# Kernel tuning notes

Hardware: AMD Instinct MI355X
Metric: run time of the kernel (lower is better)

## Reference

```python
import jax, jax.numpy as jnp
import numpy as np
import math

B, L, D_IN = 4, 8192, 64
H = 256          # d_model
N2 = 32          # d_state // 2 complex conjugate pairs (S4D)
NL = 4           # n_layers
D_OUT = 10


def setup_inputs() -> dict:
    key = jax.random.key(0)
    ks = jax.random.split(key, 16)
    x = jax.random.normal(ks[0], (B, L, D_IN), dtype=jnp.float32)
    # encoder Linear(d_input, d_model)
    enc_W = jax.random.normal(ks[1], (H, D_IN), dtype=jnp.float32) / np.sqrt(D_IN)
    enc_b = jnp.zeros((H,), dtype=jnp.float32)
    # per-layer S4D parameters (stacked over n_layers)
    log_dt = jax.random.uniform(ks[2], (NL, H), dtype=jnp.float32,
                                minval=math.log(1e-3), maxval=math.log(1e-1))
    log_A_re = jnp.full((NL, H, N2), math.log(0.5), dtype=jnp.float32)
    A_im = jnp.tile(math.pi * jnp.arange(N2, dtype=jnp.float32), (NL, H, 1))
    C_re = jax.random.normal(ks[3], (NL, H, N2), dtype=jnp.float32) * (0.5 ** 0.5)
    C_im = jax.random.normal(ks[4], (NL, H, N2), dtype=jnp.float32) * (0.5 ** 0.5)
    D = jax.random.normal(ks[5], (NL, H), dtype=jnp.float32)
    # S4 block output linear (H -> 2H) followed by GLU
    Wo = jax.random.normal(ks[6], (NL, 2 * H, H), dtype=jnp.float32) / np.sqrt(H)
    bo = jnp.zeros((NL, 2 * H), dtype=jnp.float32)
    # post-norm LayerNorm over d_model
    ln_w = jnp.ones((NL, H), dtype=jnp.float32)
    ln_b = jnp.zeros((NL, H), dtype=jnp.float32)
    # final decoder Linear(d_model, d_output)
    out_W = jax.random.normal(ks[7], (D_OUT, H), dtype=jnp.float32) / np.sqrt(H)
    out_b = jnp.zeros((D_OUT,), dtype=jnp.float32)
    return dict(x=x, enc_W=enc_W, enc_b=enc_b, log_dt=log_dt, log_A_re=log_A_re,
                A_im=A_im, C_re=C_re, C_im=C_im, D=D, Wo=Wo, bo=bo,
                ln_w=ln_w, ln_b=ln_b, out_W=out_W, out_b=out_b)


def _s4d_kernel(log_dt, log_A_re, A_im, C_re, C_im, L):
    # S4D-ZOH-ish (S4D-Lin) kernel: K[h,l] = 2 Re sum_n C~[h,n] exp(l*dt*A[h,n])
    dt = jnp.exp(log_dt)[:, None]                      # (H,1)
    A = -jnp.exp(log_A_re) + 1j * A_im                 # (H,N2)
    dtA = dt * A                                       # (H,N2)
    Ct = (C_re + 1j * C_im) * (jnp.exp(dtA) - 1.0) / A # (H,N2)
    t = jnp.arange(L, dtype=jnp.float32)
    V = jnp.exp(dtA[:, :, None] * t)                   # (H,N2,L) Vandermonde
    return 2.0 * jnp.einsum('hn,hnl->hl', Ct, V).real  # (H,L)


def reference(x, enc_W, enc_b, log_dt, log_A_re, A_im, C_re, C_im, D, Wo, bo,
              ln_w, ln_b, out_W, out_b):
    Bc, Lc, _ = x.shape
    h = x @ enc_W.T + enc_b          # (B,L,H)
    h = h.transpose(0, 2, 1)         # (B,H,L) (transposed layout)
    n_layers = log_dt.shape[0]
    for i in range(n_layers):
        K = _s4d_kernel(log_dt[i], log_A_re[i], A_im[i], C_re[i], C_im[i], Lc)
        # FFT convolution (causal, non-circular via 2L padding)
        Kf = jnp.fft.rfft(K, n=2 * Lc)                       # (H, L+1)
        hf = jnp.fft.rfft(h, n=2 * Lc)                       # (B,H,L+1)
        y = jnp.fft.irfft(hf * Kf, n=2 * Lc)[..., :Lc]
        y = y + D[i][:, None] * h                            # skip D*u
        y = jax.nn.gelu(y)
        # output linear (H -> 2H) + GLU, pointwise over length
        u = jnp.einsum('oh,bhl->bol', Wo[i], y) + bo[i][:, None]
        Hd = h.shape[1]
        z = u[:, :Hd] * jax.nn.sigmoid(u[:, Hd:])
        h = z + h                                            # residual
        # post-norm LayerNorm over channel (d_model) dim
        mu = h.mean(axis=1, keepdims=True)
        var = h.var(axis=1, keepdims=True)
        h = (h - mu) / jnp.sqrt(var + 1e-5) * ln_w[i][:, None] + ln_b[i][:, None]
    h = h.transpose(0, 2, 1)          # (B,L,H)
    return h @ out_W.T + out_b        # (B,L,d_output)
```

## Files before the change

kernel.cpp:

```cpp
#include <hip/hip_runtime.h>
#include <hip/hip_bf16.h>


constexpr int B_ = 4, L_ = 8192, DIN = 64, H_ = 256, N2_ = 32, NL_ = 4, DOUT = 10;
constexpr int LC = 64, CHK = L_ / LC;
constexpr int GCH = B_ * CHK;
constexpr int M_ = B_ * L_;

constexpr size_t OFF_WOB  = 8388608;
constexpr size_t OFF_PW   = 8650752;
constexpr size_t OFF_PCT  = 8716288;
constexpr size_t OFF_PWLC = 8781824;
constexpr size_t OFF_PZ   = 8847360;
constexpr size_t OFF_EWT  = 8912896;
constexpr size_t OFF_UCM  = 8929280;
constexpr size_t OFF_YCM  = 13123584;
constexpr size_t OFF_MT   = 21512192;
constexpr size_t OFF_MW   = 22036480;
constexpr size_t OFF_MV   = 22560768;

typedef short bf16x8 __attribute__((ext_vector_type(8)));
typedef short short8 __attribute__((ext_vector_type(8)));
typedef float f32x4  __attribute__((ext_vector_type(4)));
typedef int   int2v  __attribute__((ext_vector_type(2)));

__device__ __forceinline__ float b2f(short s) {
    union { float f; unsigned u; } c;
    c.u = ((unsigned)(unsigned short)s) << 16;
    return c.f;
}

__global__ __launch_bounds__(256) void k_params(
    const float* __restrict__ log_dt, const float* __restrict__ log_A_re,
    const float* __restrict__ A_im, const float* __restrict__ C_re,
    const float* __restrict__ C_im, float* __restrict__ ws)
{
    int idx = blockIdx.x * 256 + threadIdx.x;
    if (idx >= NL_ * H_ * N2_) return;
    int i  = idx / (H_ * N2_);
    int hh = (idx / N2_) % H_;
    float dt  = expf(log_dt[i * H_ + hh]);
    float Are = -expf(log_A_re[idx]);
    float Aim = A_im[idx];
    float zre = dt * Are, zim = dt * Aim;
    float er  = expf(zre);
    float wre = er * cosf(zim), wim = er * sinf(zim);
    float d   = Are * Are + Aim * Aim;
    float nre = wre - 1.f, nim = wim;
    float qre = (nre * Are + nim * Aim) / d;
    float qim = (nim * Are - nre * Aim) / d;
    float cr = C_re[idx], ci = C_im[idx];
    float ctre = cr * qre - ci * qim;
    float ctim = cr * qim + ci * qre;
    float er2 = expf(zre * (float)LC);
    float wlre = er2 * cosf(zim * (float)LC);
    float wlim = er2 * sinf(zim * (float)LC);
    ((float2*)(ws + OFF_PW))[idx]   = make_float2(wre, wim);
    ((float2*)(ws + OFF_PCT))[idx]  = make_float2(2.f * ctre, 2.f * ctim);
    ((float2*)(ws + OFF_PWLC))[idx] = make_float2(wlre, wlim);
    ((float2*)(ws + OFF_PZ))[idx]   = make_float2(zre, zim);
}

__global__ __launch_bounds__(256) void k_mats(const float* __restrict__ ws,
    int layer, __hip_bfloat16* __restrict__ mt, __hip_bfloat16* __restrict__ mw,
    __hip_bfloat16* __restrict__ mv)
{
    int h = blockIdx.x, tid = threadIdx.x;
    __shared__ float zre[32], zim[32], ctr[32], cti[32], kv[64];
    if (tid < 32) {
        float2 z = ((const float2*)(ws + OFF_PZ))[(size_t)layer*H_*N2_ + h*N2_ + tid];
        float2 c = ((const float2*)(ws + OFF_PCT))[(size_t)layer*H_*N2_ + h*N2_ + tid];
        zre[tid] = z.x; zim[tid] = z.y; ctr[tid] = c.x; cti[tid] = c.y;
    }
    __syncthreads();
    if (tid < 64) {
        float d = (float)tid, acc = 0.f;
        for (int n = 0; n < 32; n++) {
            float er = expf(zre[n] * d);
            float co = cosf(zim[n] * d), si = sinf(zim[n] * d);
            acc += er * (ctr[n] * co - cti[n] * si);
        }
        kv[tid] = acc;
    }
    __syncthreads();
    {
        int t = tid >> 2, j0 = (tid & 3) * 16;
        alignas(16) __hip_bfloat16 row[16];
        #pragma unroll
        for (int jj = 0; jj < 16; jj++) {
            int j = j0 + jj;
            row[jj] = __float2bfloat16(j <= t ? kv[t - j] : 0.f);
        }
        *(short8*)(mt + (size_t)h*4096 + t*64 + j0)     = *(short8*)&row[0];
        *(short8*)(mt + (size_t)h*4096 + t*64 + j0 + 8) = *(short8*)&row[8];
    }
    {
        int n = tid >> 3, j0 = (tid & 7) * 8;
        alignas(16) __hip_bfloat16 rre[8], rim[8];
        #pragma unroll
        for (int jj = 0; jj < 8; jj++) {
            float e = (float)(63 - (j0 + jj));
            float er = expf(zre[n] * e);
            rre[jj] = __float2bfloat16(er * cosf(zim[n] * e));
            rim[jj] = __float2bfloat16(er * sinf(zim[n] * e));
        }
        *(short8*)(mw + (size_t)h*4096 + (2*n)*64 + j0)   = *(short8*)&rre[0];
        *(short8*)(mw + (size_t)h*4096 + (2*n+1)*64 + j0) = *(short8*)&rim[0];
    }
    {
        int t = tid >> 2, n0 = (tid & 3) * 8;
        float e = (float)(t + 1);
        alignas(16) __hip_bfloat16 row[16];
        #pragma unroll
        for (int k = 0; k < 8; k++) {
            int n = n0 + k;
            float er = expf(zre[n] * e);
            float wr = er * cosf(zim[n] * e), wi = er * sinf(zim[n] * e);
            row[2*k]   = __float2bfloat16(ctr[n]*wr - cti[n]*wi);
            row[2*k+1] = __float2bfloat16(-(ctr[n]*wi + cti[n]*wr));
        }
        *(short8*)(mv + (size_t)h*4096 + t*64 + 2*n0)     = *(short8*)&row[0];
        *(short8*)(mv + (size_t)h*4096 + t*64 + 2*n0 + 8) = *(short8*)&row[8];
    }
}

__global__ __launch_bounds__(256) void k_transpose(const float* __restrict__ src,
    float* __restrict__ dst, int R, int Cc)
{
    __shared__ float t[32][33];
    int x = blockIdx.x * 32 + threadIdx.x;
    #pragma unroll
    for (int i = 0; i < 4; i++) {
        int yy = blockIdx.y * 32 + threadIdx.y + i * 8;
        if (x < Cc && yy < R) t[threadIdx.y + i * 8][threadIdx.x] = src[(size_t)yy * Cc + x];
    }
    __syncthreads();
    int xo = blockIdx.y * 32 + threadIdx.x;
    #pragma unroll
    for (int i = 0; i < 4; i++) {
        int yo = blockIdx.x * 32 + threadIdx.y + i * 8;
        if (xo < R && yo < Cc) dst[(size_t)yo * R + xo] = t[threadIdx.x][threadIdx.y + i * 8];
    }
}

__global__ __launch_bounds__(256) void k_wcvt(const float* __restrict__ src,
    __hip_bfloat16* __restrict__ dst, int n4)
{
    int i = blockIdx.x * 256 + threadIdx.x;
    if (i >= n4) return;
    float4 v = ((const float4*)src)[i];
    union { __hip_bfloat16 b[4]; uint2 u; } o;
    o.b[0] = __float2bfloat16(v.x); o.b[1] = __float2bfloat16(v.y);
    o.b[2] = __float2bfloat16(v.z); o.b[3] = __float2bfloat16(v.w);
    ((uint2*)dst)[i] = o.u;
}

__global__ __launch_bounds__(256) void k_encoder(const float* __restrict__ x,
    const float* __restrict__ encWT, const float* __restrict__ enc_b,
    __hip_bfloat16* __restrict__ u)
{
    __shared__ float As[DIN][36];
    __shared__ float Bs[32][268];
    int m0e = blockIdx.x * 32;
    int tid = threadIdx.x;
    const float4* x4 = (const float4*)x;
    #pragma unroll
    for (int q = 0; q < 2; q++) {
        int f = tid * 2 + q;
        int row = f >> 4, kq = f & 15;
        float4 v = x4[(size_t)(m0e + row) * 16 + kq];
        As[kq * 4 + 0][row] = v.x; As[kq * 4 + 1][row] = v.y;
        As[kq * 4 + 2][row] = v.z; As[kq * 4 + 3][row] = v.w;
    }
    int tx = tid & 31, ty = tid >> 5;
    float acc[4][8];
    #pragma unroll
    for (int p = 0; p < 4; p++)
        #pragma unroll
        for (int j = 0; j < 8; j++) acc[p][j] = 0.f;
    const float4* w4 = (const float4*)encWT;
    for (int ks = 0; ks < 2; ks++) {
        __syncthreads();
        #pragma unroll
        for (int it = 0; it < 8; it++) {
            int q = it * 256 + tid;
            int row = q >> 6, c4 = q & 63;
            *(float4*)&Bs[row][c4 * 4] = w4[ks * 2048 + q];
        }
        __syncthreads();
        #pragma unroll 8
        for (int kk = 0; kk < 32; kk++) {
            int k = ks * 32 + kk;
            float4 a  = *(const float4*)&As[k][ty * 4];
            float4 b0 = *(const float4*)&Bs[kk][tx * 4];
            float4 b1 = *(const float4*)&Bs[kk][128 + tx * 4];
            float av[4] = {a.x, a.y, a.z, a.w};
            float bv[8] = {b0.x, b0.y, b0.z, b0.w, b1.x, b1.y, b1.z, b1.w};
            #pragma unroll
            for (int p = 0; p < 4; p++)
                #pragma unroll
                for (int j = 0; j < 8; j++)
                    acc[p][j] = fmaf(av[p], bv[j], acc[p][j]);
        }
    }
    float4 eb0 = *(const float4*)&enc_b[tx * 4];
    float4 eb1 = *(const float4*)&enc_b[128 + tx * 4];
    float ebv[8] = {eb0.x, eb0.y, eb0.z, eb0.w, eb1.x, eb1.y, eb1.z, eb1.w};
    __syncthreads();
    #pragma unroll
    for (int p = 0; p < 4; p++) {
        int pl = ty * 4 + p;
        #pragma unroll
        for (int j = 0; j < 4; j++) Bs[pl][tx * 4 + j]       = acc[p][j] + ebv[j];
        #pragma unroll
        for (int j = 0; j < 4; j++) Bs[pl][128 + tx * 4 + j] = acc[p][j + 4] + ebv[j + 4];
    }
    __syncthreads();
    {
        alignas(16) __hip_bfloat16 row[32];
        #pragma unroll
        for (int pl = 0; pl < 32; pl++) row[pl] = __float2bfloat16(Bs[pl][tid]);
        #pragma unroll
        for (int q = 0; q < 4; q++)
            *(short8*)(u + (size_t)tid * M_ + m0e + q * 8) = *(short8*)&row[q * 8];
    }
}

__global__ __launch_bounds__(256) void k_ssm(const __hip_bfloat16* __restrict__ ucm,
    const __hip_bfloat16* __restrict__ mt, const __hip_bfloat16* __restrict__ mw,
    const __hip_bfloat16* __restrict__ mv, const float* __restrict__ ws, int layer,
    const float* __restrict__ Dp, __hip_bfloat16* __restrict__ ycm)
{
    __shared__ __hip_bfloat16 ulds[L_];
    __shared__ __hip_bfloat16 st[CHK * 64];
    __shared__ float segT[8][32][2];
    int h = blockIdx.x >> 2, b = blockIdx.x & 3;
    int tid = threadIdx.x, w = tid >> 6, l = tid & 63, l15 = l & 15, l4 = l >> 4;
    const __hip_bfloat16* ub = ucm + (size_t)h * M_ + (size_t)b * L_;
    #pragma unroll
    for (int it = 0; it < 4; it++) {
        int e0 = it * 2048 + tid * 8;
        short8 v = *(const short8*)(ub + e0);
        int c = e0 >> 6, e = e0 & 63;
        *(short8*)&ulds[c * 64 + (e ^ ((c & 7) << 3))] = v;
    }
    __syncthreads();
    {
        const __hip_bfloat16* bbase = mw + (size_t)h * 4096 + l15 * 64 + l4 * 8;
        #pragma unroll
        for (int half = 0; half < 2; half++) {
            int g0 = (w + half * 4) * 16;
            int ca = g0 + l15;
            f32x4 acc[4];
            #pragma unroll
            for (int nj = 0; nj < 4; nj++) acc[nj] = (f32x4)0.f;
            #pragma unroll
            for (int ks = 0; ks < 2; ks++) {
                int e = l4 * 8 + ks * 32;
                bf16x8 a = *(const bf16x8*)&ulds[ca * 64 + (e ^ ((ca & 7) << 3))];
                #pragma unroll
                for (int nj = 0; nj < 4; nj++) {
                    bf16x8 bb = *(const bf16x8*)(bbase + nj * 16 * 64 + ks * 32);
                    acc[nj] = __builtin_amdgcn_mfma_f32_16x16x32_bf16(a, bb, acc[nj], 0, 0, 0);
                }
            }
            #pragma unroll
            for (int nj = 0; nj < 4; nj++)
                #pragma unroll
                for (int r = 0; r < 4; r++) {
                    int c = g0 + l4 * 4 + r, e = nj * 16 + l15;
                    st[c * 64 + (e ^ ((c & 7) << 3))] = __float2bfloat16(acc[nj][r]);
                }
        }
    }
    __syncthreads();
    {
        int s = tid >> 5, n = tid & 31;
        float2 wl = ((const float2*)(ws + OFF_PWLC))[(size_t)layer * H_ * N2_ + h * 32 + n];
        float tr = 0.f, ti = 0.f;
        for (int j = 0; j < 16; j++) {
            int c = s * 16 + j;
            __hip_bfloat162* p = (__hip_bfloat162*)&st[c * 64 + ((2 * n) ^ ((c & 7) << 3))];
            float2 v = __bfloat1622float2(*p);
            float nr = fmaf(wl.x, tr, v.x); nr = fmaf(-wl.y, ti, nr);
            float ni = fmaf(wl.x, ti, v.y); ni = fmaf(wl.y, tr, ni);
            tr = nr; ti = ni;
        }
        segT[s][n][0] = tr; segT[s][n][1] = ti;
        __syncthreads();
        float wr = wl.x, wi = wl.y;
        #pragma unroll
        for (int q = 0; q < 4; q++) {
            float nr = wr * wr - wi * wi, ni = 2.f * wr * wi;
            wr = nr; wi = ni;
        }
        float ar = 0.f, ai = 0.f;
        for (int t = 0; t < s; t++) {
            float Tx = segT[t][n][0], Ty = segT[t][n][1];
            float nr = fmaf(wr, ar, Tx); nr = fmaf(-wi, ai, nr);
            float ni = fmaf(wr, ai, Ty); ni = fmaf(wi, ar, ni);
            ar = nr; ai = ni;
        }
        for (int j = 0; j < 16; j++) {
            int c = s * 16 + j;
            __hip_bfloat162* p = (__hip_bfloat162*)&st[c * 64 + ((2 * n) ^ ((c & 7) << 3))];
            float2 v = __bfloat1622float2(*p);
            *p = __float22bfloat162_rn(make_float2(ar, ai));
            float nr = fmaf(wl.x, ar, v.x); nr = fmaf(-wl.y, ai, nr);
            float ni = fmaf(wl.x, ai, v.y); ni = fmaf(wl.y, ar, ni);
            ar = nr; ai = ni;
        }
    }
    __syncthreads();
    {
        const __hip_bfloat16* bt = mt + (size_t)h * 4096 + l15 * 64 + l4 * 8;
        const __hip_bfloat16* bv = mv + (size_t)h * 4096 + l15 * 64 + l4 * 8;
        float Dh = Dp[layer * H_ + h];
        __hip_bfloat16* yb = ycm + (size_t)h * M_ + (size_t)b * L_;
        #pragma unroll
        for (int half = 0; half < 2; half++) {
            int g0 = (w + half * 4) * 16;
            int ca = g0 + l15;
            f32x4 acc[4];
            #pragma unroll
            for (int nj = 0; nj < 4; nj++) acc[nj] = (f32x4)0.f;
            #pragma unroll
            for (int ks = 0; ks < 2; ks++) {
                int e = l4 * 8 + ks * 32;
                bf16x8 a = *(const bf16x8*)&ulds[ca * 64 + (e ^ ((ca & 7) << 3))];
                #pragma unroll
                for (int nj = 0; nj < 4; nj++) {
                    bf16x8 bb = *(const bf16x8*)(bt + nj * 16 * 64 + ks * 32);
                    acc[nj] = __builtin_amdgcn_mfma_f32_16x16x32_bf16(a, bb, acc[nj], 0, 0, 0);
                }
            }
            #pragma unroll
            for (int ks = 0; ks < 2; ks++) {
                int e = l4 * 8 + ks * 32;
                bf16x8 a = *(const bf16x8*)&st[ca * 64 + (e ^ ((ca & 7) << 3))];
                #pragma unroll
                for (int nj = 0; nj < 4; nj++) {
                    bf16x8 bb = *(const bf16x8*)(bv + nj * 16 * 64 + ks * 32);
                    acc[nj] = __builtin_amdgcn_mfma_f32_16x16x32_bf16(a, bb, acc[nj], 0, 0, 0);
                }
            }
            #pragma unroll
            for (int nj = 0; nj < 4; nj++)
                #pragma unroll
                for (int r = 0; r < 4; r++) {
                    int g = g0 + l4 * 4 + r;
                    int e = nj * 16 + l15;
                    float uv = __bfloat162float(ulds[g * 64 + (e ^ ((g & 7) << 3))]);
                    float v = fmaf(Dh, uv, acc[nj][r]);
                    float gg = 0.7978845608028654f * fmaf(0.044715f * v, v * v, v);
                    float yv = v / (1.f + __expf(-2.f * gg));
                    yb[(size_t)g * 64 + nj * 16 + l15] = __float2bfloat16(yv);
                }
        }
    }
}

__global__ __launch_bounds__(256) void k_glu_mfma(
    const __hip_bfloat16* __restrict__ ycm,
    const __hip_bfloat16* __restrict__ wob,
    const float* __restrict__ bo, const float* __restrict__ lnw,
    const float* __restrict__ lnb,
    __hip_bfloat16* __restrict__ u)
{
    __shared__ int buf[8320];
    __shared__ float red[4][32][2];
    int* bufA = buf;
    int* bufR = buf + 4160;
    int tid = threadIdx.x;
    int w = tid >> 6, l = tid & 63, l15 = l & 15, l4 = l >> 4;
    int m0 = blockIdx.x * 32;
    int nv = w * 64;

    {
        int p = tid & 127, ph = tid >> 7;
        const __hip_bfloat16* a0p = ycm + (size_t)(2 * p) * M_ + m0 + ph * 16;
        const __hip_bfloat16* a1p = a0p + M_;
        const __hip_bfloat16* r0p = u + (size_t)(2 * p) * M_ + m0 + ph * 16;
        const __hip_bfloat16* r1p = r0p + M_;
        short8 a0a = *(const short8*)(a0p);
        short8 a0b = *(const short8*)(a0p + 8);
        short8 a1a = *(const short8*)(a1p);
        short8 a1b = *(const short8*)(a1p + 8);
        short8 r0a = *(const short8*)(r0p);
        short8 r0b = *(const short8*)(r0p + 8);
        short8 r1a = *(const short8*)(r1p);
        short8 r1b = *(const short8*)(r1p + 8);
        int* da = bufA + ph * 16 * 130 + p;
        int* dr = bufR + ph * 16 * 130 + p;
        #pragma unroll
        for (int j = 0; j < 8; j++) {
            da[j * 130]       = ((int)(unsigned short)a0a[j]) | (((int)(unsigned short)a1a[j]) << 16);
            da[(8 + j) * 130] = ((int)(unsigned short)a0b[j]) | (((int)(unsigned short)a1b[j]) << 16);
            dr[j * 130]       = ((int)(unsigned short)r0a[j]) | (((int)(unsigned short)r1a[j]) << 16);
            dr[(8 + j) * 130] = ((int)(unsigned short)r0b[j]) | (((int)(unsigned short)r1b[j]) << 16);
        }
    }
    __syncthreads();

    f32x4 accv[2][4], accg[2][4];
    #pragma unroll
    for (int sub = 0; sub < 2; sub++)
        #pragma unroll
        for (int nj = 0; nj < 4; nj++) { accv[sub][nj] = (f32x4)0.f; accg[sub][nj] = (f32x4)0.f; }

    int abase0 = l15 * 130 + l4 * 4;
    #pragma unroll 2
    for (int ks = 0; ks < 8; ks++) {
        int k0 = ks * 32 + l4 * 8;
        union { int2v d[2]; bf16x8 v; } a0u, a1u;
        a0u.d[0] = *(const int2v*)&bufA[abase0 + ks * 16];
        a0u.d[1] = *(const int2v*)&bufA[abase0 + ks * 16 + 2];
        a1u.d[0] = *(const int2v*)&bufA[abase0 + 16 * 130 + ks * 16];
        a1u.d[1] = *(const int2v*)&bufA[abase0 + 16 * 130 + ks * 16 + 2];
        bf16x8 a0 = a0u.v;
        bf16x8 a1 = a1u.v;
        #pragma unroll
        for (int nj = 0; nj < 4; nj++) {
            bf16x8 bv = *(const bf16x8*)(wob + (size_t)(nv + nj * 16 + l15) * H_ + k0);
            bf16x8 bg = *(const bf16x8*)(wob + (size_t)(256 + nv + nj * 16 + l15) * H_ + k0);
            accv[0][nj] = __builtin_amdgcn_mfma_f32_16x16x32_bf16(a0, bv, accv[0][nj], 0, 0, 0);
            accg[0][nj] = __builtin_amdgcn_mfma_f32_16x16x32_bf16(a0, bg, accg[0][nj], 0, 0, 0);
            accv[1][nj] = __builtin_amdgcn_mfma_f32_16x16x32_bf16(a1, bv, accv[1][nj], 0, 0, 0);
            accg[1][nj] = __builtin_amdgcn_mfma_f32_16x16x32_bf16(a1, bg, accg[1][nj], 0, 0, 0);
        }
    }

    float bov[4], bog[4], lw[4], lb[4];
    #pragma unroll
    for (int nj = 0; nj < 4; nj++) {
        int cn = nv + nj * 16 + l15;
        bov[nj] = bo[cn]; bog[nj] = bo[256 + cn];
        lw[nj] = lnw[cn]; lb[nj] = lnb[cn];
    }
    const short* bufRs = (const short*)bufR;
    #pragma unroll
    for (int sub = 0; sub < 2; sub++) {
        #pragma unroll
        for (int r = 0; r < 4; r++) {
            int lr = sub * 16 + l4 * 4 + r;
            float s = 0.f, ss = 0.f;
            #pragma unroll
            for (int nj = 0; nj < 4; nj++) {
                int cn = nv + nj * 16 + l15;
                float uv = accv[sub][nj][r] + bov[nj];
                float ug = accg[sub][nj][r] + bog[nj];
                float z = uv / (1.f + __expf(-ug));
                float v = z + b2f(bufRs[lr * 260 + cn]);
                accv[sub][nj][r] = v;
                s += v; ss += v * v;
            }
            #pragma unroll
            for (int off = 1; off < 16; off <<= 1) {
                s  += __shfl_xor(s, off);
                ss += __shfl_xor(ss, off);
            }
            if (l15 == 0) { red[w][lr][0] = s; red[w][lr][1] = ss; }
        }
    }
    __syncthreads();
    short* lt = (short*)buf;
    #pragma unroll
    for (int sub = 0; sub < 2; sub++) {
        #pragma unroll
        for (int r = 0; r < 4; r++) {
            int lr = sub * 16 + l4 * 4 + r;
            float s  = red[0][lr][0] + red[1][lr][0] + red[2][lr][0] + red[3][lr][0];
            float ss = red[0][lr][1] + red[1][lr][1] + red[2][lr][1] + red[3][lr][1];
            float mu = s * (1.f / 256.f);
            float var = ss * (1.f / 256.f) - mu * mu;
            float rstd = rsqrtf(var + 1e-5f);
            #pragma unroll
            for (int nj = 0; nj < 4; nj++) {
                int cn = nv + nj * 16 + l15;
                float val = (accv[sub][nj][r] - mu) * rstd * lw[nj] + lb[nj];
                __hip_bfloat16 bval = __float2bfloat16(val);
                lt[cn * 34 + lr] = *(short*)&bval;
            }
        }
    }
    __syncthreads();
    {
        #pragma unroll
        for (int q = 0; q < 4; q++)
            *(short8*)(u + (size_t)tid * M_ + m0 + q * 8)
                = *(short8*)&lt[tid * 34 + q * 8];
    }
}

__global__ __launch_bounds__(256) void k_decoder(const __hip_bfloat16* __restrict__ u,
    const float* __restrict__ out_W, const float* __restrict__ out_b,
    float* __restrict__ out)
{
    __shared__ float hs[64][260];
    __shared__ float wl[10][260];
    int m0 = blockIdx.x * 64;
    int tid = threadIdx.x;
    {
        const __hip_bfloat16* src = u + (size_t)tid * M_ + m0;
        bf16x8 raw[8];
        #pragma unroll
        for (int q = 0; q < 8; q++) raw[q] = *(const bf16x8*)(src + q * 8);
        #pragma unroll
        for (int p = 0; p < 64; p++)
            hs[p][tid] = b2f(raw[p >> 3][p & 7]);
    }
    for (int q = tid; q < 640; q += 256) {
        int r = q / 64, k4 = q % 64;
        *(float4*)&wl[r][k4 * 4] = ((const float4*)out_W)[q];
    }
    __syncthreads();
    int slot = tid & 15;
    if (slot < DOUT) {
        #pragma unroll
        for (int pass = 0; pass < 4; pass++) {
            int pl = pass * 16 + (tid >> 4);
            float a0 = 0.f, a1 = 0.f, a2 = 0.f, a3 = 0.f;
            #pragma unroll 8
            for (int k = 0; k < 256; k += 4) {
                a0 = fmaf(hs[pl][k + 0], wl[slot][k + 0], a0);
                a1 = fmaf(hs[pl][k + 1], wl[slot][k + 1], a1);
                a2 = fmaf(hs[pl][k + 2], wl[slot][k + 2], a2);
                a3 = fmaf(hs[pl][k + 3], wl[slot][k + 3], a3);
            }
            out[(size_t)(m0 + pl) * DOUT + slot] = (a0 + a1) + (a2 + a3) + out_b[slot];
        }
    }
}

extern "C" void kernel_launch(void* const* d_in, const int* in_sizes, int n_in,
                              void* d_out, int out_size, void* d_ws, size_t ws_size,
                              hipStream_t stream)
{
    (void)in_sizes; (void)n_in; (void)out_size; (void)ws_size;
    const float* x        = (const float*)d_in[0];
    const float* enc_W    = (const float*)d_in[1];
    const float* enc_b    = (const float*)d_in[2];
    const float* log_dt   = (const float*)d_in[3];
    const float* log_A_re = (const float*)d_in[4];
    const float* A_im     = (const float*)d_in[5];
    const float* C_re     = (const float*)d_in[6];
    const float* C_im     = (const float*)d_in[7];
    const float* Dp       = (const float*)d_in[8];
    const float* Wo       = (const float*)d_in[9];
    const float* bo       = (const float*)d_in[10];
    const float* lnw      = (const float*)d_in[11];
    const float* lnb      = (const float*)d_in[12];
    const float* out_W    = (const float*)d_in[13];
    const float* out_b    = (const float*)d_in[14];
    float* ws = (float*)d_ws;
    __hip_bfloat16* u   = (__hip_bfloat16*)(ws + OFF_UCM);
    __hip_bfloat16* ycm = (__hip_bfloat16*)(ws + OFF_YCM);
    __hip_bfloat16* mt = (__hip_bfloat16*)(ws + OFF_MT);
    __hip_bfloat16* mw = (__hip_bfloat16*)(ws + OFF_MW);
    __hip_bfloat16* mv = (__hip_bfloat16*)(ws + OFF_MV);
    __hip_bfloat16* wob = (__hip_bfloat16*)(ws + OFF_WOB);

    k_params<<<NL_ * H_ * N2_ / 256, 256, 0, stream>>>(log_dt, log_A_re, A_im, C_re, C_im, ws);
    dim3 tb(32, 8);
    k_transpose<<<dim3(DIN / 32, H_ / 32), tb, 0, stream>>>(enc_W, ws + OFF_EWT, H_, DIN);
    k_wcvt<<<(NL_ * 2 * H_ * H_ / 4 + 255) / 256, 256, 0, stream>>>(Wo, wob, NL_ * 2 * H_ * H_ / 4);
    k_encoder<<<M_ / 32, 256, 0, stream>>>(x, ws + OFF_EWT, enc_b, u);
    for (int i = 0; i < NL_; i++) {
        k_mats<<<H_, 256, 0, stream>>>(ws, i, mt, mw, mv);
        k_ssm<<<H_ * B_, 256, 0, stream>>>(u, mt, mw, mv, ws, i, Dp, ycm);
        k_glu_mfma<<<M_ / 32, 256, 0, stream>>>(ycm,
            wob + (size_t)i * 2 * H_ * H_, bo + (size_t)i * 2 * H_,
            lnw + (size_t)i * H_, lnb + (size_t)i * H_, u);
    }
    k_decoder<<<M_ / 64, 256, 0, stream>>>(u, out_W, out_b, (float*)d_out);
}
```

Measured before the change: 449.1 us.

## Process two row tiles per GLU block with prefetched loads; repack decoder staging

The GLU/LayerNorm kernel now handles 64 rows per block as two 32-row tiles. The second tile's activations and residuals are loaded into registers ahead of time, so global memory latency overlaps the first tile's MFMA and epilogue work. Launching half as many blocks also halves the redundant weight reads per row. Separately, the decoder stages its input as packed bf16 pairs in shared memory instead of fp32, which halves LDS use and changes how the dot-product reads it. The cost is more registers per thread and less parallelism across blocks.

```diff
diff --git a/kernel.cpp b/kernel.cpp
--- a/kernel.cpp
+++ b/kernel.cpp
@@ -373,62 +373,19 @@
     int* bufR = buf + 4160;
     int tid = threadIdx.x;
     int w = tid >> 6, l = tid & 63, l15 = l & 15, l4 = l >> 4;
-    int m0 = blockIdx.x * 32;
+    int mb = blockIdx.x * 64;
     int nv = w * 64;
-
-    {
-        int p = tid & 127, ph = tid >> 7;
-        const __hip_bfloat16* a0p = ycm + (size_t)(2 * p) * M_ + m0 + ph * 16;
-        const __hip_bfloat16* a1p = a0p + M_;
-        const __hip_bfloat16* r0p = u + (size_t)(2 * p) * M_ + m0 + ph * 16;
-        const __hip_bfloat16* r1p = r0p + M_;
-        short8 a0a = *(const short8*)(a0p);
-        short8 a0b = *(const short8*)(a0p + 8);
-        short8 a1a = *(const short8*)(a1p);
-        short8 a1b = *(const short8*)(a1p + 8);
-        short8 r0a = *(const short8*)(r0p);
-        short8 r0b = *(const short8*)(r0p + 8);
-        short8 r1a = *(const short8*)(r1p);
-        short8 r1b = *(const short8*)(r1p + 8);
-        int* da = bufA + ph * 16 * 130 + p;
-        int* dr = bufR + ph * 16 * 130 + p;
-        #pragma unroll
-        for (int j = 0; j < 8; j++) {
-            da[j * 130]       = ((int)(unsigned short)a0a[j]) | (((int)(unsigned short)a1a[j]) << 16);
-            da[(8 + j) * 130] = ((int)(unsigned short)a0b[j]) | (((int)(unsigned short)a1b[j]) << 16);
-            dr[j * 130]       = ((int)(unsigned short)r0a[j]) | (((int)(unsigned short)r1a[j]) << 16);
-            dr[(8 + j) * 130] = ((int)(unsigned short)r0b[j]) | (((int)(unsigned short)r1b[j]) << 16);
-        }
-    }
-    __syncthreads();
-
-    f32x4 accv[2][4], accg[2][4];
-    #pragma unroll
-    for (int sub = 0; sub < 2; sub++)
-        #pragma unroll
-        for (int nj = 0; nj < 4; nj++) { accv[sub][nj] = (f32x4)0.f; accg[sub][nj] = (f32x4)0.f; }
-
-    int abase0 = l15 * 130 + l4 * 4;
-    #pragma unroll 2
-    for (int ks = 0; ks < 8; ks++) {
-        int k0 = ks * 32 + l4 * 8;
-        union { int2v d[2]; bf16x8 v; } a0u, a1u;
-        a0u.d[0] = *(const int2v*)&bufA[abase0 + ks * 16];
-        a0u.d[1] = *(const int2v*)&bufA[abase0 + ks * 16 + 2];
-        a1u.d[0] = *(const int2v*)&bufA[abase0 + 16 * 130 + ks * 16];
-        a1u.d[1] = *(const int2v*)&bufA[abase0 + 16 * 130 + ks * 16 + 2];
-        bf16x8 a0 = a0u.v;
-        bf16x8 a1 = a1u.v;
-        #pragma unroll
-        for (int nj = 0; nj < 4; nj++) {
-            bf16x8 bv = *(const bf16x8*)(wob + (size_t)(nv + nj * 16 + l15) * H_ + k0);
-            bf16x8 bg = *(const bf16x8*)(wob + (size_t)(256 + nv + nj * 16 + l15) * H_ + k0);
-            accv[0][nj] = __builtin_amdgcn_mfma_f32_16x16x32_bf16(a0, bv, accv[0][nj], 0, 0, 0);
-            accg[0][nj] = __builtin_amdgcn_mfma_f32_16x16x32_bf16(a0, bg, accg[0][nj], 0, 0, 0);
-            accv[1][nj] = __builtin_amdgcn_mfma_f32_16x16x32_bf16(a1, bv, accv[1][nj], 0, 0, 0);
-            accg[1][nj] = __builtin_amdgcn_mfma_f32_16x16x32_bf16(a1, bg, accg[1][nj], 0, 0, 0);
-        }
-    }
+    int p = tid & 127, ph = tid >> 7;
+    const __hip_bfloat16* aB = ycm + (size_t)(2 * p) * M_ + mb + ph * 16;
+    const __hip_bfloat16* rB = u + (size_t)(2 * p) * M_ + mb + ph * 16;
+
+    short8 A0[4], R0[4], A1[4], R1[4];
+    A0[0] = *(const short8*)(aB);          A0[1] = *(const short8*)(aB + 8);
+    A0[2] = *(const short8*)(aB + M_);     A0[3] = *(const short8*)(aB + M_ + 8);
+    R0[0] = *(const short8*)(rB);          R0[1] = *(const short8*)(rB + 8);
+    R0[2] = *(const short8*)(rB + M_);     R0[3] = *(const short8*)(rB + M_ + 8);
+    A1[0] = *(const short8*)(aB + 32);     A1[1] = *(const short8*)(aB + 40);
+    A1[2] = *(const short8*)(aB + M_ + 32);A1[3] = *(const short8*)(aB + M_ + 40);
 
     float bov[4], bog[4], lw[4], lb[4];
     #pragma unroll
@@ -437,58 +394,119 @@
         bov[nj] = bo[cn]; bog[nj] = bo[256 + cn];
         lw[nj] = lnw[cn]; lb[nj] = lnb[cn];
     }
-    const short* bufRs = (const short*)bufR;
-    #pragma unroll
-    for (int sub = 0; sub < 2; sub++) {
-        #pragma unroll
-        for (int r = 0; r < 4; r++) {
-            int lr = sub * 16 + l4 * 4 + r;
-            float s = 0.f, ss = 0.f;
+
+    {
+        int* da = bufA + ph * 16 * 130 + p;
+        int* dr = bufR + ph * 16 * 130 + p;
+        #pragma unroll
+        for (int j = 0; j < 8; j++) {
+            da[j * 130]       = ((int)(unsigned short)A0[0][j]) | (((int)(unsigned short)A0[2][j]) << 16);
+            da[(8 + j) * 130] = ((int)(unsigned short)A0[1][j]) | (((int)(unsigned short)A0[3][j]) << 16);
+            dr[j * 130]       = ((int)(unsigned short)R0[0][j]) | (((int)(unsigned short)R0[2][j]) << 16);
+            dr[(8 + j) * 130] = ((int)(unsigned short)R0[1][j]) | (((int)(unsigned short)R0[3][j]) << 16);
+        }
+    }
+    __syncthreads();
+
+    int abase0 = l15 * 130 + l4 * 4;
+    #pragma unroll
+    for (int tile = 0; tile < 2; tile++) {
+        int m0 = mb + tile * 32;
+        f32x4 accv[2][4], accg[2][4];
+        #pragma unroll
+        for (int sub = 0; sub < 2; sub++)
+            #pragma unroll
+            for (int nj = 0; nj < 4; nj++) { accv[sub][nj] = (f32x4)0.f; accg[sub][nj] = (f32x4)0.f; }
+
+        #pragma unroll 2
+        for (int ks = 0; ks < 8; ks++) {
+            int k0 = ks * 32 + l4 * 8;
+            union { int2v d[2]; bf16x8 v; } a0u, a1u;
+            a0u.d[0] = *(const int2v*)&bufA[abase0 + ks * 16];
+            a0u.d[1] = *(const int2v*)&bufA[abase0 + ks * 16 + 2];
+            a1u.d[0] = *(const int2v*)&bufA[abase0 + 16 * 130 + ks * 16];
+            a1u.d[1] = *(const int2v*)&bufA[abase0 + 16 * 130 + ks * 16 + 2];
+            bf16x8 a0 = a0u.v;
+            bf16x8 a1 = a1u.v;
             #pragma unroll
             for (int nj = 0; nj < 4; nj++) {
-                int cn = nv + nj * 16 + l15;
-                float uv = accv[sub][nj][r] + bov[nj];
-                float ug = accg[sub][nj][r] + bog[nj];
-                float z = uv / (1.f + __expf(-ug));
-                float v = z + b2f(bufRs[lr * 260 + cn]);
-                accv[sub][nj][r] = v;
-                s += v; ss += v * v;
-            }
-            #pragma unroll
-            for (int off = 1; off < 16; off <<= 1) {
-                s  += __shfl_xor(s, off);
-                ss += __shfl_xor(ss, off);
-            }
-            if (l15 == 0) { red[w][lr][0] = s; red[w][lr][1] = ss; }
-        }
-    }
-    __syncthreads();
-    short* lt = (short*)buf;
-    #pragma unroll
-    for (int sub = 0; sub < 2; sub++) {
-        #pragma unroll
-        for (int r = 0; r < 4; r++) {
-            int lr = sub * 16 + l4 * 4 + r;
-            float s  = red[0][lr][0] + red[1][lr][0] + red[2][lr][0] + red[3][lr][0];
-            float ss = red[0][lr][1] + red[1][lr][1] + red[2][lr][1] + red[3][lr][1];
-            float mu = s * (1.f / 256.f);
-            float var = ss * (1.f / 256.f) - mu * mu;
-            float rstd = rsqrtf(var + 1e-5f);
-            #pragma unroll
-            for (int nj = 0; nj < 4; nj++) {
-                int cn = nv + nj * 16 + l15;
-                float val = (accv[sub][nj][r] - mu) * rstd * lw[nj] + lb[nj];
-                __hip_bfloat16 bval = __float2bfloat16(val);
-                lt[cn * 34 + lr] = *(short*)&bval;
-            }
-        }
-    }
-    __syncthreads();
-    {
+                bf16x8 bv = *(const bf16x8*)(wob + (size_t)(nv + nj * 16 + l15) * H_ + k0);
+                bf16x8 bg = *(const bf16x8*)(wob + (size_t)(256 + nv + nj * 16 + l15) * H_ + k0);
+                accv[0][nj] = __builtin_amdgcn_mfma_f32_16x16x32_bf16(a0, bv, accv[0][nj], 0, 0, 0);
+                accg[0][nj] = __builtin_amdgcn_mfma_f32_16x16x32_bf16(a0, bg, accg[0][nj], 0, 0, 0);
+                accv[1][nj] = __builtin_amdgcn_mfma_f32_16x16x32_bf16(a1, bv, accv[1][nj], 0, 0, 0);
+                accg[1][nj] = __builtin_amdgcn_mfma_f32_16x16x32_bf16(a1, bg, accg[1][nj], 0, 0, 0);
+            }
+        }
+
+        const short* bufRs = (const short*)bufR;
+        #pragma unroll
+        for (int sub = 0; sub < 2; sub++) {
+            #pragma unroll
+            for (int r = 0; r < 4; r++) {
+                int lr = sub * 16 + l4 * 4 + r;
+                float s = 0.f, ss = 0.f;
+                #pragma unroll
+                for (int nj = 0; nj < 4; nj++) {
+                    int cn = nv + nj * 16 + l15;
+                    float uv = accv[sub][nj][r] + bov[nj];
+                    float ug = accg[sub][nj][r] + bog[nj];
+                    float z = uv / (1.f + __expf(-ug));
+                    float v = z + b2f(bufRs[lr * 260 + cn]);
+                    accv[sub][nj][r] = v;
+                    s += v; ss += v * v;
+                }
+                #pragma unroll
+                for (int off = 1; off < 16; off <<= 1) {
+                    s  += __shfl_xor(s, off);
+                    ss += __shfl_xor(ss, off);
+                }
+                if (l15 == 0) { red[w][lr][0] = s; red[w][lr][1] = ss; }
+            }
+        }
+        if (tile == 0) {
+            R1[0] = *(const short8*)(rB + 32);      R1[1] = *(const short8*)(rB + 40);
+            R1[2] = *(const short8*)(rB + M_ + 32); R1[3] = *(const short8*)(rB + M_ + 40);
+        }
+        __syncthreads();
+        short* lt = (short*)buf;
+        #pragma unroll
+        for (int sub = 0; sub < 2; sub++) {
+            #pragma unroll
+            for (int r = 0; r < 4; r++) {
+                int lr = sub * 16 + l4 * 4 + r;
+                float s  = red[0][lr][0] + red[1][lr][0] + red[2][lr][0] + red[3][lr][0];
+                float ss = red[0][lr][1] + red[1][lr][1] + red[2][lr][1] + red[3][lr][1];
+                float mu = s * (1.f / 256.f);
+                float var = ss * (1.f / 256.f) - mu * mu;
+                float rstd = rsqrtf(var + 1e-5f);
+                #pragma unroll
+                for (int nj = 0; nj < 4; nj++) {
+                    int cn = nv + nj * 16 + l15;
+                    float val = (accv[sub][nj][r] - mu) * rstd * lw[nj] + lb[nj];
+                    __hip_bfloat16 bval = __float2bfloat16(val);
+                    lt[cn * 34 + lr] = *(short*)&bval;
+                }
+            }
+        }
+        __syncthreads();
         #pragma unroll
         for (int q = 0; q < 4; q++)
             *(short8*)(u + (size_t)tid * M_ + m0 + q * 8)
                 = *(short8*)&lt[tid * 34 + q * 8];
+        if (tile == 0) {
+            __syncthreads();
+            int* da = bufA + ph * 16 * 130 + p;
+            int* dr = bufR + ph * 16 * 130 + p;
+            #pragma unroll
+            for (int j = 0; j < 8; j++) {
+                da[j * 130]       = ((int)(unsigned short)A1[0][j]) | (((int)(unsigned short)A1[2][j]) << 16);
+                da[(8 + j) * 130] = ((int)(unsigned short)A1[1][j]) | (((int)(unsigned short)A1[3][j]) << 16);
+                dr[j * 130]       = ((int)(unsigned short)R1[0][j]) | (((int)(unsigned short)R1[2][j]) << 16);
+                dr[(8 + j) * 130] = ((int)(unsigned short)R1[1][j]) | (((int)(unsigned short)R1[3][j]) << 16);
+            }
+            __syncthreads();
+        }
     }
 }
 
@@ -496,18 +514,27 @@
     const float* __restrict__ out_W, const float* __restrict__ out_b,
     float* __restrict__ out)
 {
-    __shared__ float hs[64][260];
+    __shared__ int ds[64 * 130];
     __shared__ float wl[10][260];
     int m0 = blockIdx.x * 64;
     int tid = threadIdx.x;
     {
-        const __hip_bfloat16* src = u + (size_t)tid * M_ + m0;
-        bf16x8 raw[8];
-        #pragma unroll
-        for (int q = 0; q < 8; q++) raw[q] = *(const bf16x8*)(src + q * 8);
-        #pragma unroll
-        for (int p = 0; p < 64; p++)
-            hs[p][tid] = b2f(raw[p >> 3][p & 7]);
+        int p = tid & 127, ph = tid >> 7;
+        const __hip_bfloat16* s0 = u + (size_t)(2 * p) * M_ + m0 + ph * 32;
+        const __hip_bfloat16* s1 = s0 + M_;
+        short8 y0[4], y1[4];
+        #pragma unroll
+        for (int q = 0; q < 4; q++) {
+            y0[q] = *(const short8*)(s0 + q * 8);
+            y1[q] = *(const short8*)(s1 + q * 8);
+        }
+        int* dst = ds + (ph * 32) * 130 + p;
+        #pragma unroll
+        for (int q = 0; q < 4; q++)
+            #pragma unroll
+            for (int j = 0; j < 8; j++)
+                dst[(q * 8 + j) * 130] =
+                    ((int)(unsigned short)y0[q][j]) | (((int)(unsigned short)y1[q][j]) << 16);
     }
     for (int q = tid; q < 640; q += 256) {
         int r = q / 64, k4 = q % 64;
@@ -519,15 +546,15 @@
         #pragma unroll
         for (int pass = 0; pass < 4; pass++) {
             int pl = pass * 16 + (tid >> 4);
-            float a0 = 0.f, a1 = 0.f, a2 = 0.f, a3 = 0.f;
+            const int* row = ds + pl * 130;
+            float a0 = 0.f, a1 = 0.f;
             #pragma unroll 8
-            for (int k = 0; k < 256; k += 4) {
-                a0 = fmaf(hs[pl][k + 0], wl[slot][k + 0], a0);
-                a1 = fmaf(hs[pl][k + 1], wl[slot][k + 1], a1);
-                a2 = fmaf(hs[pl][k + 2], wl[slot][k + 2], a2);
-                a3 = fmaf(hs[pl][k + 3], wl[slot][k + 3], a3);
-            }
-            out[(size_t)(m0 + pl) * DOUT + slot] = (a0 + a1) + (a2 + a3) + out_b[slot];
+            for (int d = 0; d < 128; d++) {
+                int v = row[d];
+                a0 = fmaf(b2f((short)(v & 0xffff)),  wl[slot][2 * d],     a0);
+                a1 = fmaf(b2f((short)(v >> 16)),     wl[slot][2 * d + 1], a1);
+            }
+            out[(size_t)(m0 + pl) * DOUT + slot] = a0 + a1 + out_b[slot];
         }
     }
 }
@@ -568,7 +595,7 @@
     for (int i = 0; i < NL_; i++) {
         k_mats<<<H_, 256, 0, stream>>>(ws, i, mt, mw, mv);
         k_ssm<<<H_ * B_, 256, 0, stream>>>(u, mt, mw, mv, ws, i, Dp, ycm);
-        k_glu_mfma<<<M_ / 32, 256, 0, stream>>>(ycm,
+        k_glu_mfma<<<M_ / 64, 256, 0, stream>>>(ycm,
             wob + (size_t)i * 2 * H_ * H_, bo + (size_t)i * 2 * H_,
             lnw + (size_t)i * H_, lnb + (size_t)i * H_, u);
     }
```

New measurement: 418.8 us. 1.07x faster.
